# Optimization experiments

Hardware: AMD Instinct MI355X
Metric: run time of the kernel (lower is better)

## Reference

```python
import jax, jax.numpy as jnp
import numpy as np

HEADS = 16
DIM_HEAD = 64
SCALE = DIM_HEAD ** -0.5


def setup_inputs() -> dict:
    key = jax.random.key(0)
    k1, k2, k3, k4 = jax.random.split(key, 4)
    b, n, dim = 2, 2048, 1024
    inner = HEADS * DIM_HEAD  # 1024
    x = jax.random.normal(k1, (b, n, dim), dtype=jnp.float32)
    mask = jax.random.randint(k2, (b, n), 0, 2, dtype=jnp.int32)
    Wqkv = jax.random.normal(k3, (dim, inner), dtype=jnp.float32) * (dim ** -0.5)
    Wout = jax.random.normal(k4, (inner, dim), dtype=jnp.float32) * (inner ** -0.5)
    bout = jnp.zeros((dim,), dtype=jnp.float32)
    return {"x": x, "mask": mask, "Wqkv": Wqkv, "Wout": Wout, "bout": bout}


def reference(x, mask, Wqkv, Wout, bout):
    b, n, _ = x.shape
    # shared projection: w acts as q = k = v (CRATE subspace attention)
    w = jnp.einsum('bnd,de->bne', x, Wqkv)
    w = w.reshape(b, n, HEADS, DIM_HEAD).transpose(0, 2, 1, 3)  # b h n d
    dots = jnp.einsum('bhid,bhjd->bhij', w, w) * SCALE           # b h n n
    attn = jax.nn.softmax(dots, axis=-1)
    # post-softmax multiplicative masking (mask=1 zeros the column)
    m = mask[:, None, None, :].astype(attn.dtype)
    attn = attn * (1.0 - m)
    out = jnp.einsum('bhij,bhjd->bhid', attn, w)                 # b h n d
    out = out.transpose(0, 2, 1, 3).reshape(b, n, HEADS * DIM_HEAD)
    return jnp.einsum('bne,ed->bnd', out, Wout) + bout
```

## Files before the change

kernel.cpp:

```cpp
#include <hip/hip_runtime.h>
#include <hip/hip_bf16.h>
#include <stdint.h>

typedef unsigned short u16;
typedef unsigned int u32;
typedef __bf16 bf16x8 __attribute__((ext_vector_type(8)));
typedef float f32x4 __attribute__((ext_vector_type(4)));
typedef float f32x16 __attribute__((ext_vector_type(16)));
typedef u32 u32x4 __attribute__((ext_vector_type(4)));

#define AS1 __attribute__((address_space(1)))
#define AS3 __attribute__((address_space(3)))

__device__ __forceinline__ void async16(const u16* g, u16* l) {
  __builtin_amdgcn_global_load_lds((const AS1 uint32_t*)(const void*)g,
                                   (AS3 uint32_t*)l, 16, 0, 0);
}

__device__ __forceinline__ u16 f2bf(float v) {
  union { __hip_bfloat16 b; u16 u; } c; c.b = __float2bfloat16(v); return c.u;
}

__device__ __forceinline__ u32 pkbf(float a, float b) {
  u32 r;
  asm("v_cvt_pk_bf16_f32 %0, %1, %2" : "=v"(r) : "v"(a), "v"(b));
  return r;
}

__device__ __forceinline__ void swap32(u32 &a, u32 &b) {
  asm("v_permlane32_swap_b32 %0, %1" : "+v"(a), "+v"(b));
}

#if __has_builtin(__builtin_amdgcn_exp2f)
#define fast_exp2(x) __builtin_amdgcn_exp2f(x)
#else
#define fast_exp2(x) exp2f(x)
#endif

#if __has_builtin(__builtin_amdgcn_rcpf)
#define fast_rcp(x) __builtin_amdgcn_rcpf(x)
#else
#define fast_rcp(x) (1.0f / (x))
#endif

__device__ __forceinline__ uint4 pack8(float4 lo, float4 hi) {
  uint4 q;
  q.x = (u32)f2bf(lo.x) | ((u32)f2bf(lo.y) << 16);
  q.y = (u32)f2bf(lo.z) | ((u32)f2bf(lo.w) << 16);
  q.z = (u32)f2bf(hi.x) | ((u32)f2bf(hi.y) << 16);
  q.w = (u32)f2bf(hi.z) | ((u32)f2bf(hi.w) << 16);
  return q;
}

__global__ void prep(const float* __restrict__ x, u16* __restrict__ xb,
                     const float* __restrict__ Wqkv, u16* __restrict__ WqkvT,
                     const float* __restrict__ Wout, u16* __restrict__ WoutT) {
  const int tx = threadIdx.x, ty = threadIdx.y, z = blockIdx.z;
  if (z >= 2) {
    const int cid = (z - 2) * 256 + blockIdx.y * 16 + blockIdx.x;
    const int t = ty * 16 + tx;
    const int i = (cid * 256 + t) * 8;
    float4 lo = *(const float4*)(x + i);
    float4 hi = *(const float4*)(x + i + 4);
    *(uint4*)(xb + i) = pack8(lo, hi);
    return;
  }
  const float* in = z ? Wout : Wqkv;
  u16* out = z ? WoutT : WqkvT;
  __shared__ u16 tile[64][65];
  const int c0 = blockIdx.x * 64, r0 = blockIdx.y * 64;
#pragma unroll
  for (int i = 0; i < 4; i++) {
    const int row = r0 + ty + i * 16;
    float4 v = *(const float4*)&in[(size_t)row * 1024 + c0 + tx * 4];
    tile[tx * 4 + 0][ty + i * 16] = f2bf(v.x);
    tile[tx * 4 + 1][ty + i * 16] = f2bf(v.y);
    tile[tx * 4 + 2][ty + i * 16] = f2bf(v.z);
    tile[tx * 4 + 3][ty + i * 16] = f2bf(v.w);
  }
  __syncthreads();
#pragma unroll
  for (int i = 0; i < 4; i++) {
    const int orow = c0 + ty + i * 16;
    u32 w0 = (u32)tile[ty + i * 16][tx * 4 + 0] | ((u32)tile[ty + i * 16][tx * 4 + 1] << 16);
    u32 w1 = (u32)tile[ty + i * 16][tx * 4 + 2] | ((u32)tile[ty + i * 16][tx * 4 + 3] << 16);
    uint2 pk = {w0, w1};
    *(uint2*)&out[(size_t)orow * 1024 + r0 + tx * 4] = pk;
  }
}

__global__ void scale_transpose_v(const u16* __restrict__ w, const int* __restrict__ mask,
                                  u16* __restrict__ Vt) {
  __shared__ u16 tile[64][65];
  const int tx = threadIdx.x, ty = threadIdx.y;
  const int j0 = blockIdx.x * 64;
  const int bh = blockIdx.z, b = bh >> 4, hc = (bh & 15) * 64;
#pragma unroll
  for (int i = 0; i < 4; i++) {
    const int j = j0 + ty + i * 16;
    uint2 v = *(const uint2*)&w[(size_t)(b * 2048 + j) * 1024 + hc + tx * 4];
    if (mask[b * 2048 + j]) { v.x = 0u; v.y = 0u; }
    tile[tx * 4 + 0][ty + i * 16] = (u16)(v.x & 0xFFFF);
    tile[tx * 4 + 1][ty + i * 16] = (u16)(v.x >> 16);
    tile[tx * 4 + 2][ty + i * 16] = (u16)(v.y & 0xFFFF);
    tile[tx * 4 + 3][ty + i * 16] = (u16)(v.y >> 16);
  }
  __syncthreads();
#pragma unroll
  for (int i = 0; i < 4; i++) {
    const int d = ty + i * 16;
    u32 w0 = (u32)tile[d][tx * 4 + 0] | ((u32)tile[d][tx * 4 + 1] << 16);
    u32 w1 = (u32)tile[d][tx * 4 + 2] | ((u32)tile[d][tx * 4 + 3] << 16);
    uint2 pk = {w0, w1};
    *(uint2*)&Vt[((size_t)bh * 64 + d) * 2048 + j0 + tx * 4] = pk;
  }
}

template<bool OUT_F32>
__launch_bounds__(256)
__global__ void gemm_bt(const u16* __restrict__ A, const u16* __restrict__ BT,
                        void* __restrict__ Cp, const float* __restrict__ bias,
                        int M, int N, int K) {
  __shared__ __align__(16) u16 As[2][64 * 64];
  __shared__ __align__(16) u16 Bs[2][64 * 64];
  const int t = threadIdx.x;
  const int lane = t & 63, wave = t >> 6;
  const int ql = lane & 31, hi = lane >> 5, swz = ql & 7;
  const int wgid = blockIdx.x + gridDim.x * blockIdx.y;
  const int c = wgid & 7, ii = wgid >> 3;
  const int m0 = (c * 8 + (ii & 7)) * 64;
  const int n0 = (ii >> 3) * 64;
  const int wm = (wave & 1) * 32, wn = (wave >> 1) * 32;

  f32x16 acc = {};

  const int sr = t >> 3;
  const int sc8 = ((t & 7) ^ (sr & 7)) * 8;
  const u16* gAt = A + (size_t)(m0 + sr) * K + sc8;
  const u16* gBt = BT + (size_t)(n0 + sr) * K + sc8;

#define GSTAGE(buf, k0s) do { \
    async16(gAt + (k0s),                   &As[buf][t * 8]); \
    async16(gAt + (k0s) + (size_t)32 * K,  &As[buf][t * 8 + 2048]); \
    async16(gBt + (k0s),                   &Bs[buf][t * 8]); \
    async16(gBt + (k0s) + (size_t)32 * K,  &Bs[buf][t * 8 + 2048]); \
  } while (0)

  GSTAGE(0, 0);

  int cur = 0;
  for (int k0 = 0; k0 < K; k0 += 64) {
    if (k0 + 64 < K) {
      GSTAGE(cur ^ 1, k0 + 64);
      asm volatile("s_waitcnt vmcnt(4)" ::: "memory");
    } else {
      asm volatile("s_waitcnt vmcnt(0)" ::: "memory");
    }
    __builtin_amdgcn_s_barrier();
    __builtin_amdgcn_sched_barrier(0);

#pragma unroll
    for (int kk = 0; kk < 4; kk++) {
      bf16x8 af = *(const bf16x8*)&As[cur][(wm + ql) * 64 + (((2 * kk + hi) ^ swz) * 8)];
      bf16x8 bfr = *(const bf16x8*)&Bs[cur][(wn + ql) * 64 + (((2 * kk + hi) ^ swz) * 8)];
      acc = __builtin_amdgcn_mfma_f32_32x32x16_bf16(af, bfr, acc, 0, 0, 0);
    }
    asm volatile("s_waitcnt lgkmcnt(0)" ::: "memory");
    __builtin_amdgcn_sched_barrier(0);
    __builtin_amdgcn_s_barrier();
    __builtin_amdgcn_sched_barrier(0);
    cur ^= 1;
  }
#undef GSTAGE

  const float bv = bias ? bias[n0 + wn + ql] : 0.f;
  const int col = n0 + wn + ql;

#pragma unroll
  for (int r = 0; r < 16; r++) {
    const int row = m0 + wm + (r & 3) + 8 * (r >> 2) + 4 * hi;
    const size_t ci = (size_t)row * N + col;
    const float v = acc[r] + bv;
    if (OUT_F32) ((float*)Cp)[ci] = v;
    else ((u16*)Cp)[ci] = f2bf(v);
  }
}

#define C1 0.18033688f
#define C2 -28.853901f
__launch_bounds__(512)
__global__ void attn_kernel(const u16* __restrict__ w, const u16* __restrict__ Vt,
                            u16* __restrict__ y) {
  __shared__ __align__(16) u16 Ks[2][2][32 * 64];
  __shared__ __align__(16) u16 Vs[2][2][64 * 32];
  const int t = threadIdx.x, lane = t & 63, wv = t >> 6;
  const int qg = wv & 3, kgr = wv >> 2;
  const int ql = lane & 31, hi = lane >> 5, swz = ql & 7, vswz = ql & 3;
  const int wgid = blockIdx.x + 16 * blockIdx.y;
  const int newid = (wgid & 7) * 64 + (wgid >> 3);
  const int bh = newid >> 4, b = bh >> 4, hc = (bh & 15) * 64;
  const int q0 = (newid & 15) * 128;
  const size_t rowb = (size_t)b * 2048;

  const int tt = t & 255;
  const int sg = t >> 8;
  const int skey = tt >> 3;
  const int scl = ((tt & 7) ^ (skey & 7)) * 8;
  const int vd = tt >> 2;
  const int vcl = ((tt & 3) ^ (vd & 3)) * 8;
  const int sjb = sg * 1024;
  const u16* kptr = w + rowb * 1024 + hc;
  const u16* vptr = Vt + (size_t)bh * 64 * 2048;

  bf16x8 qf[4];
  {
    const size_t qrow = rowb + q0 + qg * 32 + ql;
#pragma unroll
    for (int ks = 0; ks < 4; ks++)
      qf[ks] = *(const bf16x8*)&w[qrow * 1024 + hc + ks * 16 + hi * 8];
  }

  union { u32x4 u; bf16x8 bf; } ones;
  ones.u = (u32x4){0x3F803F80u, 0x3F803F80u, 0x3F803F80u, 0x3F803F80u};

  f32x16 o0 = {}, o1 = {};
  f32x16 den = {};

#define STAGE(buf, j0s) do { \
    async16(kptr + (size_t)(sjb + (j0s) + skey) * 1024 + scl, &Ks[sg][buf][tt * 8]); \
    async16(vptr + (size_t)vd * 2048 + sjb + (j0s) + vcl,     &Vs[sg][buf][tt * 8]); \
  } while (0)

  STAGE(0, 0);
  __syncthreads();

  int cur = 0;
  for (int j0 = 0; j0 < 1024; j0 += 32) {
    if (j0 + 32 < 1024) STAGE(cur ^ 1, j0 + 32);

    const u16* Wt = Ks[kgr][cur];
    const u16* Vts = Vs[kgr][cur];

    f32x16 p = {};
#pragma unroll
    for (int ks = 0; ks < 4; ks++) {
      bf16x8 af = *(const bf16x8*)&Wt[ql * 64 + (((ks * 2 + hi) ^ swz) * 8)];
      p = __builtin_amdgcn_mfma_f32_32x32x16_bf16(af, qf[ks], p, 0, 0, 0);
    }
    float e[16];
#pragma unroll
    for (int r = 0; r < 16; r++)
      e[r] = fast_exp2(fmaf(p[r], C1, C2));
    u32 a0 = pkbf(e[0], e[1]),   b0 = pkbf(e[4], e[5]);   swap32(a0, b0);
    u32 a1 = pkbf(e[2], e[3]),   b1 = pkbf(e[6], e[7]);   swap32(a1, b1);
    u32 a2 = pkbf(e[8], e[9]),   b2 = pkbf(e[12], e[13]); swap32(a2, b2);
    u32 a3 = pkbf(e[10], e[11]), b3 = pkbf(e[14], e[15]); swap32(a3, b3);
    u32x4 pa0 = {a0, a1, b0, b1};
    u32x4 pa1 = {a2, a3, b2, b3};

    __builtin_amdgcn_s_setprio(1);
    {
      union { u32x4 u; bf16x8 bf; } c0, c1; c0.u = pa0; c1.u = pa1;
      bf16x8 v00 = *(const bf16x8*)&Vts[ql * 32 + ((hi ^ vswz) * 8)];
      bf16x8 v01 = *(const bf16x8*)&Vts[(32 + ql) * 32 + ((hi ^ vswz) * 8)];
      bf16x8 v10 = *(const bf16x8*)&Vts[ql * 32 + (((2 + hi) ^ vswz) * 8)];
      bf16x8 v11 = *(const bf16x8*)&Vts[(32 + ql) * 32 + (((2 + hi) ^ vswz) * 8)];
      o0 = __builtin_amdgcn_mfma_f32_32x32x16_bf16(c0.bf, v00, o0, 0, 0, 0);
      o1 = __builtin_amdgcn_mfma_f32_32x32x16_bf16(c0.bf, v01, o1, 0, 0, 0);
      den = __builtin_amdgcn_mfma_f32_32x32x16_bf16(c0.bf, ones.bf, den, 0, 0, 0);
      o0 = __builtin_amdgcn_mfma_f32_32x32x16_bf16(c1.bf, v10, o0, 0, 0, 0);
      o1 = __builtin_amdgcn_mfma_f32_32x32x16_bf16(c1.bf, v11, o1, 0, 0, 0);
      den = __builtin_amdgcn_mfma_f32_32x32x16_bf16(c1.bf, ones.bf, den, 0, 0, 0);
    }
    __builtin_amdgcn_s_setprio(0);

    __syncthreads();
    cur ^= 1;
  }
#undef STAGE

  float* mrg = (float*)Ks;
  float* slot = mrg + (qg * 64 + lane) * 17;
  f32x16 om0 = o0, om1 = o1, dm = den;
#define MERGE(vec) do { \
    if (kgr == 1) { \
      _Pragma("unroll") for (int r = 0; r < 16; r++) slot[r] = (vec)[r]; \
    } \
    __syncthreads(); \
    if (kgr == 0) { \
      _Pragma("unroll") for (int r = 0; r < 16; r++) (vec)[r] += slot[r]; \
    } \
    __syncthreads(); \
  } while (0)
  MERGE(om0);
  MERGE(om1);
  MERGE(dm);
#undef MERGE

  if (kgr == 0) {
#pragma unroll
    for (int r = 0; r < 16; r++) {
      const int qo = (r & 3) + 8 * (r >> 2) + 4 * hi;
      const float iv = fast_rcp(dm[r]);
      const size_t orow = rowb + q0 + qg * 32 + qo;
      y[orow * 1024 + hc + ql]      = f2bf(om0[r] * iv);
      y[orow * 1024 + hc + 32 + ql] = f2bf(om1[r] * iv);
    }
  }
}

extern "C" void kernel_launch(void* const* d_in, const int* in_sizes, int n_in,
                              void* d_out, int out_size, void* d_ws, size_t ws_size,
                              hipStream_t stream) {
  const float* x    = (const float*)d_in[0];
  const int* mask   = (const int*)d_in[1];
  const float* Wqkv = (const float*)d_in[2];
  const float* Wout = (const float*)d_in[3];
  const float* bout = (const float*)d_in[4];
  float* out = (float*)d_out;

  u16* w     = (u16*)d_ws;
  u16* y     = w + 4096 * 1024;
  u16* WqkvT = y + 4096 * 1024;
  u16* WoutT = WqkvT + 1024 * 1024;
  u16* Vt    = WoutT + 1024 * 1024;
  u16* xb    = y;

  prep<<<dim3(16, 16, 10), dim3(16, 16), 0, stream>>>(x, xb, Wqkv, WqkvT, Wout, WoutT);
  gemm_bt<false><<<dim3(64, 16), 256, 0, stream>>>(xb, WqkvT, w, nullptr, 4096, 1024, 1024);
  scale_transpose_v<<<dim3(32, 1, 32), dim3(16, 16), 0, stream>>>(w, mask, Vt);
  attn_kernel<<<dim3(16, 32), 512, 0, stream>>>(w, Vt, y);
  gemm_bt<true><<<dim3(64, 16), 256, 0, stream>>>(y, WoutT, out, bout, 4096, 1024, 1024);
}
```

Measured before the change: 160.5 us.

## Split attention key range four ways with 64-query blocks and doubled grid

Reorganizes the attention workgroup from 4 query groups by 2 key groups (128 queries each) to 2 query groups by 4 key groups (64 queries each), doubling the grid to 1024 workgroups. Each wave now processes 512 keys instead of 1024, and the final merge sums three partial accumulators through shared memory. The intent is more workgroups to fill the CUs and shorter serial loops per wave. The cost is doubled K/V loading per query, larger LDS staging buffers, and a heavier cross-wave reduction.

```diff
diff --git a/kernel.cpp b/kernel.cpp
--- a/kernel.cpp
+++ b/kernel.cpp
@@ -191,24 +191,23 @@
 __launch_bounds__(512)
 __global__ void attn_kernel(const u16* __restrict__ w, const u16* __restrict__ Vt,
                             u16* __restrict__ y) {
-  __shared__ __align__(16) u16 Ks[2][2][32 * 64];
-  __shared__ __align__(16) u16 Vs[2][2][64 * 32];
+  __shared__ __align__(16) u16 Ks[4][2][32 * 64];
+  __shared__ __align__(16) u16 Vs[4][2][64 * 32];
   const int t = threadIdx.x, lane = t & 63, wv = t >> 6;
-  const int qg = wv & 3, kgr = wv >> 2;
+  const int qg = wv & 1, kgr = wv >> 1;
   const int ql = lane & 31, hi = lane >> 5, swz = ql & 7, vswz = ql & 3;
-  const int wgid = blockIdx.x + 16 * blockIdx.y;
-  const int newid = (wgid & 7) * 64 + (wgid >> 3);
-  const int bh = newid >> 4, b = bh >> 4, hc = (bh & 15) * 64;
-  const int q0 = (newid & 15) * 128;
+  const int wgid = blockIdx.x + 32 * blockIdx.y;
+  const int newid = (wgid & 7) * 128 + (wgid >> 3);
+  const int bh = newid >> 5, b = bh >> 4, hc = (bh & 15) * 64;
+  const int q0 = (newid & 31) * 64;
   const size_t rowb = (size_t)b * 2048;
 
-  const int tt = t & 255;
-  const int sg = t >> 8;
-  const int skey = tt >> 3;
-  const int scl = ((tt & 7) ^ (skey & 7)) * 8;
-  const int vd = tt >> 2;
-  const int vcl = ((tt & 3) ^ (vd & 3)) * 8;
-  const int sjb = sg * 1024;
+  const int sA = t & 255;
+  const int kgA = t >> 8, kgB = kgA + 2;
+  const int rowK = sA >> 3;
+  const int chK = ((sA & 7) ^ (rowK & 7)) * 8;
+  const int dV = sA >> 2;
+  const int chV = ((sA & 3) ^ (dV & 3)) * 8;
   const u16* kptr = w + rowb * 1024 + hc;
   const u16* vptr = Vt + (size_t)bh * 64 * 2048;
 
@@ -227,16 +226,18 @@
   f32x16 den = {};
 
 #define STAGE(buf, j0s) do { \
-    async16(kptr + (size_t)(sjb + (j0s) + skey) * 1024 + scl, &Ks[sg][buf][tt * 8]); \
-    async16(vptr + (size_t)vd * 2048 + sjb + (j0s) + vcl,     &Vs[sg][buf][tt * 8]); \
+    async16(kptr + (size_t)(kgA * 512 + (j0s) + rowK) * 1024 + chK, &Ks[kgA][buf][sA * 8]); \
+    async16(kptr + (size_t)(kgB * 512 + (j0s) + rowK) * 1024 + chK, &Ks[kgB][buf][sA * 8]); \
+    async16(vptr + (size_t)dV * 2048 + kgA * 512 + (j0s) + chV,     &Vs[kgA][buf][sA * 8]); \
+    async16(vptr + (size_t)dV * 2048 + kgB * 512 + (j0s) + chV,     &Vs[kgB][buf][sA * 8]); \
   } while (0)
 
   STAGE(0, 0);
   __syncthreads();
 
   int cur = 0;
-  for (int j0 = 0; j0 < 1024; j0 += 32) {
-    if (j0 + 32 < 1024) STAGE(cur ^ 1, j0 + 32);
+  for (int j0 = 0; j0 < 512; j0 += 32) {
+    if (j0 + 32 < 512) STAGE(cur ^ 1, j0 + 32);
 
     const u16* Wt = Ks[kgr][cur];
     const u16* Vts = Vs[kgr][cur];
@@ -280,15 +281,18 @@
 #undef STAGE
 
   float* mrg = (float*)Ks;
-  float* slot = mrg + (qg * 64 + lane) * 17;
   f32x16 om0 = o0, om1 = o1, dm = den;
 #define MERGE(vec) do { \
-    if (kgr == 1) { \
-      _Pragma("unroll") for (int r = 0; r < 16; r++) slot[r] = (vec)[r]; \
+    if (kgr > 0) { \
+      float* sw = mrg + ((qg * 3 + (kgr - 1)) * 64 + lane) * 17; \
+      _Pragma("unroll") for (int r = 0; r < 16; r++) sw[r] = (vec)[r]; \
     } \
     __syncthreads(); \
     if (kgr == 0) { \
-      _Pragma("unroll") for (int r = 0; r < 16; r++) (vec)[r] += slot[r]; \
+      _Pragma("unroll") for (int ws = 0; ws < 3; ws++) { \
+        float* s2 = mrg + ((qg * 3 + ws) * 64 + lane) * 17; \
+        _Pragma("unroll") for (int r = 0; r < 16; r++) (vec)[r] += s2[r]; \
+      } \
     } \
     __syncthreads(); \
   } while (0)
@@ -329,6 +333,6 @@
   prep<<<dim3(16, 16, 10), dim3(16, 16), 0, stream>>>(x, xb, Wqkv, WqkvT, Wout, WoutT);
   gemm_bt<false><<<dim3(64, 16), 256, 0, stream>>>(xb, WqkvT, w, nullptr, 4096, 1024, 1024);
   scale_transpose_v<<<dim3(32, 1, 32), dim3(16, 16), 0, stream>>>(w, mask, Vt);
-  attn_kernel<<<dim3(16, 32), 512, 0, stream>>>(w, Vt, y);
+  attn_kernel<<<dim3(32, 32), 512, 0, stream>>>(w, Vt, y);
   gemm_bt<true><<<dim3(64, 16), 256, 0, stream>>>(y, WoutT, out, bout, 4096, 1024, 1024);
 }
```

New measurement: 166.5 us. 3.7% more time.
